# Optimization experiments

Hardware: AMD Instinct MI355X
Metric: run time of the kernel (lower is better)

Reference implementation:

```python
import jax, jax.numpy as jnp
import numpy as np

N_NODES = 50000
N_EDGES = 800000
DIM = 64
N_LAYERS = 5


def setup_inputs() -> dict:
    key = jax.random.key(0)
    k1, k2, k3, k4, k5 = jax.random.split(key, 5)
    x = jax.random.normal(k1, (N_NODES, DIM), dtype=jnp.float32)
    # 3 weight matrices per GIN layer (2 hidden + 1 output Dense, all [dim,dim], relu, no bias)
    W = jax.random.normal(k2, (N_LAYERS, 3, DIM, DIM), dtype=jnp.float32) * (1.0 / np.sqrt(DIM))
    # per-layer read-out Dense(1, use_bias=False)
    Wl = jax.random.normal(k3, (N_LAYERS, DIM), dtype=jnp.float32) * (1.0 / np.sqrt(DIM))
    src = jax.random.randint(k4, (N_EDGES,), 0, N_NODES, dtype=jnp.int32)
    dst = jax.random.randint(k5, (N_EDGES,), 0, N_NODES, dtype=jnp.int32)
    return {"x": x, "W": W, "Wl": Wl, "src": src, "dst": dst}


def reference(x, W, Wl, src, dst):
    n = x.shape[0]
    h = x
    pooled = []  # per-layer global mean pool  [dim]
    for i in range(N_LAYERS):
        agg = h + jax.ops.segment_sum(h[src], dst, num_segments=n)  # (1+eps)*h + sum_neighbors
        h = jax.nn.relu(agg @ W[i, 0])
        h = jax.nn.relu(h @ W[i, 1])
        h = jax.nn.relu(h @ W[i, 2])
        pooled.append(jnp.mean(h, axis=0))
    # stack per-layer Dense(1) read-outs, sum over layers, sigmoid -> shape [1]
    logits = jnp.einsum("ld,ld->l", jnp.stack(pooled), Wl)  # [5]
    return jax.nn.sigmoid(jnp.sum(logits)[None])
```

## Files before the change

kernel.cpp:

```cpp
#include <hip/hip_runtime.h>
#include <hip/hip_fp16.h>
#include <math.h>

#define N_NODES 50000
#define N_EDGES 800000
#define DIM 64
#define N_LAYERS 5

#define BLK 128
#define ROWS 32
#define HSTRIDE 68
#define POOL_REP 16

#define CAP 64
#define NROW_PAD 50016

#define BF_BLOCKS 512
#define EPB2 ((N_EDGES + BF_BLOCKS - 1) / BF_BLOCKS)

#define WFRAG_PER_LAYER (3 * 2 * 4 * 64 * 8)
#define XP (N_NODES * DIM / 4)
#define WP (N_LAYERS * WFRAG_PER_LAYER)
#define PREP_BLOCKS ((XP + WP) / 256)

typedef __attribute__((ext_vector_type(8))) short short8;
typedef __attribute__((ext_vector_type(8))) unsigned short ushort8_t;
typedef __attribute__((ext_vector_type(4))) float floatx4;

__device__ inline unsigned short bf16_rne(float f) {
    unsigned int u = __float_as_uint(f);
    return (unsigned short)((u + 0x7FFFu + ((u >> 16) & 1u)) >> 16);
}
__device__ inline float e5m2_f32(unsigned char b) {
    return __half2float(__ushort_as_half((unsigned short)((unsigned short)b << 8)));
}
__device__ inline unsigned char f32_e5m2(float f) {
    unsigned short us = __half_as_ushort(__float2half(f));
    us = (unsigned short)(us + 0x7F + ((us >> 8) & 1));
    return (unsigned char)(us >> 8);
}
__device__ inline __half2 e5m2x2_lo(unsigned d) {
    unsigned h = __builtin_amdgcn_perm(0u, d, 0x01050004u);
    return __builtin_bit_cast(__half2, h);
}
__device__ inline __half2 e5m2x2_hi(unsigned d) {
    unsigned h = __builtin_amdgcn_perm(0u, d, 0x03070206u);
    return __builtin_bit_cast(__half2, h);
}

__global__ __launch_bounds__(256) void setup_kernel(const float* __restrict__ x,
                                                    const float* __restrict__ W,
                                                    const int* __restrict__ src,
                                                    const int* __restrict__ dst,
                                                    unsigned char* __restrict__ x8,
                                                    unsigned short* __restrict__ wfrag,
                                                    int* __restrict__ rowCnt,
                                                    unsigned short* __restrict__ ell) {
    int b = blockIdx.x;
    const int t = threadIdx.x;
    if (b < PREP_BLOCKS) {
        int i = b * 256 + t;
        if (i < XP) {
            float4 v = ((const float4*)x)[i];
            uchar4 u;
            u.x = f32_e5m2(v.x); u.y = f32_e5m2(v.y);
            u.z = f32_e5m2(v.z); u.w = f32_e5m2(v.w);
            ((uchar4*)x8)[i] = u;
        } else {
            int tt = i - XP;
            int j    = tt & 7;
            int lane = (tt >> 3) & 63;
            int nt   = (tt >> 9) & 3;
            int kt   = (tt >> 11) & 1;
            int rest = tt >> 12;
            int p    = rest % 3;
            int layer= rest / 3;
            int k = kt * 32 + (lane >> 4) * 8 + j;
            int n = nt * 16 + (lane & 15);
            float v = W[(((size_t)layer * 3 + p) * 64 + k) * 64 + n];
            wfrag[tt] = bf16_rne(v);
        }
        return;
    }
    b -= PREP_BLOCKS;
    const int e0 = b * EPB2;
    for (int i = t; i < EPB2; i += 256) {
        int e = e0 + i;
        if (e < N_EDGES) {
            int d = dst[e];
            int pos = atomicAdd(&rowCnt[d], 1);
            if (pos < CAP)
                ell[(size_t)d * CAP + pos] = (unsigned short)src[e];
        }
    }
}

__global__ __launch_bounds__(BLK) void layer_kernel(const unsigned char* __restrict__ h8,
                                                    const int* __restrict__ rowCnt,
                                                    const unsigned short* __restrict__ ell,
                                                    const unsigned short* __restrict__ wf,
                                                    unsigned char* __restrict__ h_out,
                                                    float* __restrict__ pooled) {
    __shared__ float H[ROWS * HSTRIDE];
    const int tid  = threadIdx.x;
    const int lane = tid & 63;
    const int w    = __builtin_amdgcn_readfirstlane(tid >> 6);
    const int n0   = blockIdx.x * ROWS;
    const int nw   = n0 + w * 16;
    const int o8   = (lane & 7) << 3;
    const int rg   = lane >> 3;

    const int cv = rowCnt[nw + (lane & 15)];

    for (int g = 0; g < 2; ++g) {
        const int myrow = g * 8 + rg;
        const int deg = min(__shfl(cv, myrow, 64), CAP);
        int Rm = deg;
        Rm = max(Rm, __shfl_xor(Rm, 8, 64));
        Rm = max(Rm, __shfl_xor(Rm, 16, 64));
        Rm = max(Rm, __shfl_xor(Rm, 32, 64));
        const int Rpad = (Rm + 7) & ~7;
        const int rowq = nw + myrow;
        const int rq6  = rowq << 6;
        const unsigned short* ep = ell + ((size_t)rowq << 6);

        __half2 a01 = __float2half2_rn(0.f);
        __half2 a23 = a01, a45 = a01, a67 = a01;

        for (int i = 0; i < Rpad; i += 8) {
            ushort8_t ev = *(const ushort8_t*)(ep + i);
            uint2 dv[8];
            #pragma unroll
            for (int k = 0; k < 8; ++k) {
                int s6 = ((int)ev[k]) << 6;
                s6 = (i + k < deg) ? s6 : rq6;
                dv[k] = *(const uint2*)(h8 + (unsigned)(s6 | o8));
            }
            #pragma unroll
            for (int k = 0; k < 8; ++k) {
                a01 = __hadd2(a01, e5m2x2_lo(dv[k].x));
                a23 = __hadd2(a23, e5m2x2_hi(dv[k].x));
                a45 = __hadd2(a45, e5m2x2_lo(dv[k].y));
                a67 = __hadd2(a67, e5m2x2_hi(dv[k].y));
            }
        }

        uint2 sd = *(const uint2*)(h8 + (unsigned)(rq6 | o8));
        float scale = (float)(1 - (Rpad - deg));
        float2 f01 = __half22float2(a01), f23 = __half22float2(a23);
        float2 f45 = __half22float2(a45), f67 = __half22float2(a67);
        float4 r0, r1;
        r0.x = f01.x + e5m2_f32((unsigned char)(sd.x      )) * scale;
        r0.y = f01.y + e5m2_f32((unsigned char)(sd.x >>  8)) * scale;
        r0.z = f23.x + e5m2_f32((unsigned char)(sd.x >> 16)) * scale;
        r0.w = f23.y + e5m2_f32((unsigned char)(sd.x >> 24)) * scale;
        r1.x = f45.x + e5m2_f32((unsigned char)(sd.y      )) * scale;
        r1.y = f45.y + e5m2_f32((unsigned char)(sd.y >>  8)) * scale;
        r1.z = f67.x + e5m2_f32((unsigned char)(sd.y >> 16)) * scale;
        r1.w = f67.y + e5m2_f32((unsigned char)(sd.y >> 24)) * scale;
        if (rowq >= N_NODES) {
            r0.x = 0.f; r0.y = 0.f; r0.z = 0.f; r0.w = 0.f;
            r1.x = 0.f; r1.y = 0.f; r1.z = 0.f; r1.w = 0.f;
        }
        float* hp = &H[(w * 16 + myrow) * HSTRIDE + o8];
        *(float4*)hp = r0;
        *(float4*)(hp + 4) = r1;
    }
    asm volatile("s_waitcnt lgkmcnt(0)" ::: "memory");

    const int mrow = lane & 15;
    const int quad = lane >> 4;
    const short8* Bf = (const short8*)wf;

    for (int p = 0; p < 3; ++p) {
        short8 Ahi[2];
        #pragma unroll
        for (int kt = 0; kt < 2; ++kt) {
            const float* ap = &H[(w * 16 + mrow) * HSTRIDE + kt * 32 + quad * 8];
            float4 f0 = *(const float4*)ap;
            float4 f1 = *(const float4*)(ap + 4);
            float fv[8] = {f0.x, f0.y, f0.z, f0.w, f1.x, f1.y, f1.z, f1.w};
            short8 hi;
            #pragma unroll
            for (int jj = 0; jj < 8; ++jj)
                hi[jj] = (short)bf16_rne(fv[jj]);
            Ahi[kt] = hi;
        }

        floatx4 acc[4];
        #pragma unroll
        for (int nt = 0; nt < 4; ++nt) { acc[nt][0]=0.f; acc[nt][1]=0.f; acc[nt][2]=0.f; acc[nt][3]=0.f; }

        #pragma unroll
        for (int nt = 0; nt < 4; ++nt) {
            #pragma unroll
            for (int kt = 0; kt < 2; ++kt) {
                int fbase = ((p * 2 + kt) * 4 + nt) * 64 + lane;
                short8 bhi = Bf[fbase];
                acc[nt] = __builtin_amdgcn_mfma_f32_16x16x32_bf16(Ahi[kt], bhi, acc[nt], 0, 0, 0);
            }
        }
        #pragma unroll
        for (int nt = 0; nt < 4; ++nt) {
            #pragma unroll
            for (int reg = 0; reg < 4; ++reg) {
                int row = w * 16 + quad * 4 + reg;
                H[row * HSTRIDE + nt * 16 + mrow] = fmaxf(acc[nt][reg], 0.f);
            }
        }
    }
    __syncthreads();

    #pragma unroll
    for (int i = 0; i < 4; ++i) {
        int t4 = tid + i * BLK;
        int r  = t4 >> 4;
        int c  = (t4 & 15) << 2;
        int grow = n0 + r;
        if (grow < N_NODES) {
            float4 v = *(const float4*)&H[r * HSTRIDE + c];
            uchar4 u;
            u.x = f32_e5m2(v.x); u.y = f32_e5m2(v.y);
            u.z = f32_e5m2(v.z); u.w = f32_e5m2(v.w);
            *(uchar4*)(h_out + (size_t)grow * DIM + c) = u;
        }
    }

    if (tid < 64) {
        float s = 0.f;
        #pragma unroll
        for (int r = 0; r < ROWS; ++r)
            s += H[r * HSTRIDE + tid];
        atomicAdd(&pooled[(blockIdx.x & (POOL_REP - 1)) * DIM + tid], s);
    }
}

__global__ void finalize_kernel(const float* __restrict__ pooled,
                                const float* __restrict__ Wl,
                                float* __restrict__ out) {
    int c = threadIdx.x;
    float s = 0.f;
    #pragma unroll
    for (int l = 0; l < N_LAYERS; ++l) {
        float col = 0.f;
        #pragma unroll
        for (int r = 0; r < POOL_REP; ++r)
            col += pooled[(l * POOL_REP + r) * DIM + c];
        s += col * Wl[l * DIM + c];
    }
    #pragma unroll
    for (int off = 32; off > 0; off >>= 1)
        s += __shfl_down(s, off, 64);
    if (c == 0) {
        float logit = s / (float)N_NODES;
        out[0] = 1.f / (1.f + expf(-logit));
    }
}

extern "C" void kernel_launch(void* const* d_in, const int* in_sizes, int n_in,
                              void* d_out, int out_size, void* d_ws, size_t ws_size,
                              hipStream_t stream) {
    const float* x   = (const float*)d_in[0];
    const float* W   = (const float*)d_in[1];
    const float* Wl  = (const float*)d_in[2];
    const int*   src = (const int*)d_in[3];
    const int*   dst = (const int*)d_in[4];
    float* out = (float*)d_out;

    char* ws = (char*)d_ws;
    const size_t h8Bytes = (size_t)N_NODES * DIM;
    unsigned char* hX = (unsigned char*)(ws);
    unsigned char* hA = (unsigned char*)(ws + h8Bytes);
    unsigned char* hB = (unsigned char*)(ws + 2 * h8Bytes);
    unsigned short* ell = (unsigned short*)(ws + 3 * h8Bytes);
    int*   rowCnt   = (int*)(ell + (size_t)NROW_PAD * CAP);
    float* pooled   = (float*)(rowCnt + NROW_PAD);
    unsigned short* wfrag = (unsigned short*)(pooled + N_LAYERS * POOL_REP * DIM);

    hipMemsetAsync(rowCnt, 0, (NROW_PAD + N_LAYERS * POOL_REP * DIM) * sizeof(int), stream);

    setup_kernel<<<PREP_BLOCKS + BF_BLOCKS, 256, 0, stream>>>(x, W, src, dst, hX, wfrag, rowCnt, ell);

    const unsigned char* hcur = hX;
    unsigned char* hnext = hA;
    const int grid = (N_NODES + ROWS - 1) / ROWS;
    for (int l = 0; l < N_LAYERS; ++l) {
        layer_kernel<<<grid, BLK, 0, stream>>>(
            hcur, rowCnt, ell, wfrag + (size_t)l * WFRAG_PER_LAYER, hnext,
            pooled + (size_t)l * POOL_REP * DIM);
        hcur = hnext;
        hnext = (hnext == hA) ? hB : hA;
    }
    finalize_kernel<<<1, 64, 0, stream>>>(pooled, Wl, out);
}
```

Before: 203.9 us.

## Build ELL adjacency via two-pass bucketed binning with shared-memory row tiles

Replaces the per-edge global atomic scatter into the ELL array with a two-stage build. Edges are first binned into 256-row buckets using shared-memory counts and one global atomic per bucket per block. A new kernel then scatters each bucket into a shared-memory tile and writes it out with coalesced 16-byte stores. This is meant to cut random global atomics and scattered 2-byte writes, at the cost of an extra kernel launch, an intermediate edge buffer, and a fixed per-bucket capacity (CAPB) that could overflow for skewed graphs.

```diff
diff --git a/kernel.cpp b/kernel.cpp
--- a/kernel.cpp
+++ b/kernel.cpp
@@ -13,8 +13,9 @@
 #define POOL_REP 16
 
 #define CAP 64
-#define NROW_PAD 50016
-
+#define NB 196
+#define NROW_PAD (NB * 256)
+#define CAPB 5632
 #define BF_BLOCKS 512
 #define EPB2 ((N_EDGES + BF_BLOCKS - 1) / BF_BLOCKS)
 
@@ -54,8 +55,10 @@
                                                     const int* __restrict__ dst,
                                                     unsigned char* __restrict__ x8,
                                                     unsigned short* __restrict__ wfrag,
-                                                    int* __restrict__ rowCnt,
-                                                    unsigned short* __restrict__ ell) {
+                                                    int* __restrict__ bucketCnt,
+                                                    int* __restrict__ ebuf) {
+    __shared__ int cnt[NB];
+    __shared__ int basev[NB];
     int b = blockIdx.x;
     const int t = threadIdx.x;
     if (b < PREP_BLOCKS) {
@@ -84,15 +87,57 @@
     }
     b -= PREP_BLOCKS;
     const int e0 = b * EPB2;
+    for (int j = t; j < NB; j += 256) cnt[j] = 0;
+    __syncthreads();
+    for (int i = t; i < EPB2; i += 256) {
+        int e = e0 + i;
+        if (e < N_EDGES) atomicAdd(&cnt[dst[e] >> 8], 1);
+    }
+    __syncthreads();
+    for (int j = t; j < NB; j += 256) {
+        int c = cnt[j];
+        basev[j] = c ? atomicAdd(&bucketCnt[j], c) : 0;
+        cnt[j] = 0;
+    }
+    __syncthreads();
     for (int i = t; i < EPB2; i += 256) {
         int e = e0 + i;
         if (e < N_EDGES) {
             int d = dst[e];
-            int pos = atomicAdd(&rowCnt[d], 1);
-            if (pos < CAP)
-                ell[(size_t)d * CAP + pos] = (unsigned short)src[e];
-        }
-    }
+            int bb = d >> 8;
+            int pos = atomicAdd(&cnt[bb], 1);
+            ebuf[(size_t)bb * CAPB + basev[bb] + pos] = ((d & 255) << 16) | src[e];
+        }
+    }
+}
+
+__global__ __launch_bounds__(512) void bell_kernel(const int* __restrict__ ebuf,
+                                                   const int* __restrict__ bucketCnt,
+                                                   int* __restrict__ rowCnt,
+                                                   unsigned short* __restrict__ ell) {
+    __shared__ int cur[256];
+    __shared__ unsigned short tile[256 * CAP];
+    const int t = threadIdx.x;
+    const int b = blockIdx.x;
+    const int cnt_b = min(bucketCnt[b], CAPB);
+    const int* __restrict__ ereg = ebuf + (size_t)b * CAPB;
+
+    if (t < 256) cur[t] = 0;
+    __syncthreads();
+    for (int i = t; i < cnt_b; i += 512) {
+        int e = ereg[i];
+        int r = (e >> 16) & 255;
+        int pos = atomicAdd(&cur[r], 1);
+        if (pos < CAP)
+            tile[r * CAP + pos] = (unsigned short)(e & 0xFFFF);
+    }
+    __syncthreads();
+    if (t < 256) rowCnt[b * 256 + t] = min(cur[t], CAP);
+    uint4* eo = (uint4*)(ell + (size_t)b * 256 * CAP);
+    const uint4* ti = (const uint4*)tile;
+    #pragma unroll
+    for (int j = 0; j < 4; ++j)
+        eo[t + j * 512] = ti[t + j * 512];
 }
 
 __global__ __launch_bounds__(BLK) void layer_kernel(const unsigned char* __restrict__ h8,
@@ -273,13 +318,16 @@
     unsigned char* hA = (unsigned char*)(ws + h8Bytes);
     unsigned char* hB = (unsigned char*)(ws + 2 * h8Bytes);
     unsigned short* ell = (unsigned short*)(ws + 3 * h8Bytes);
-    int*   rowCnt   = (int*)(ell + (size_t)NROW_PAD * CAP);
-    float* pooled   = (float*)(rowCnt + NROW_PAD);
+    int*   ebuf     = (int*)(ell + (size_t)NROW_PAD * CAP);
+    int*   rowCnt   = ebuf + (size_t)NB * CAPB;
+    int*   bucketCnt= rowCnt + NROW_PAD;
+    float* pooled   = (float*)(bucketCnt + 256);
     unsigned short* wfrag = (unsigned short*)(pooled + N_LAYERS * POOL_REP * DIM);
 
-    hipMemsetAsync(rowCnt, 0, (NROW_PAD + N_LAYERS * POOL_REP * DIM) * sizeof(int), stream);
-
-    setup_kernel<<<PREP_BLOCKS + BF_BLOCKS, 256, 0, stream>>>(x, W, src, dst, hX, wfrag, rowCnt, ell);
+    hipMemsetAsync(bucketCnt, 0, (256 + N_LAYERS * POOL_REP * DIM) * sizeof(int), stream);
+
+    setup_kernel<<<PREP_BLOCKS + BF_BLOCKS, 256, 0, stream>>>(x, W, src, dst, hX, wfrag, bucketCnt, ebuf);
+    bell_kernel<<<NB, 512, 0, stream>>>(ebuf, bucketCnt, rowCnt, ell);
 
     const unsigned char* hcur = hX;
     unsigned char* hnext = hA;
```

Measured after the change: 181.4 us. 1.12x faster.
